# Performance work log

Measured on AMD Instinct MI355X. Metric: run time of the kernel, lower is better.

The kernel has to match this reference:

```python
import jax, jax.numpy as jnp
import numpy as np

TAU = 0.5


def _l2norm(x):
    # F.normalize(p=2, dim=1): x / max(||x||, eps) with eps=1e-12
    n = jnp.sqrt(jnp.sum(x * x, axis=1, keepdims=True))
    return x / jnp.maximum(n, 1e-12)


def setup_inputs() -> dict:
    key = jax.random.key(0)
    k1, k2 = jax.random.split(key)
    N, D = 8192, 512
    left = jax.random.normal(k1, (N, D), dtype=jnp.float32)
    right = jax.random.normal(k2, (N, D), dtype=jnp.float32)
    return {"left": left, "right": right}


def reference(left, right) -> jnp.ndarray:
    zl = _l2norm(left)
    zr = _l2norm(right)
    # [N, N] cosine-similarity matrices
    refl_sim = jnp.exp(jnp.matmul(zl, zl.T) / TAU)
    between_sim = jnp.exp(jnp.matmul(zl, zr.T) / TAU)
    between_diag = jnp.diagonal(between_sim)
    refl_diag = jnp.diagonal(refl_sim)
    denom = refl_sim.sum(axis=1) + between_sim.sum(axis=1) - refl_diag
    loss = -jnp.log(between_diag / denom)  # [N]
    return loss
```

## Files before the change

kernel.cpp:

```cpp
#include <hip/hip_runtime.h>

#define NROWS 8192
#define DDIM 512
#define ZROWS 16384
#define BM 256
#define BN 256
#define BK 64
#define KTILES (DDIM / BK)
#define NLR_BLOCKS 1024
#define NSYM_BLOCKS 528
#define NBLOCKS (NLR_BLOCKS + NSYM_BLOCKS)

typedef __attribute__((ext_vector_type(8))) short short8;
typedef __attribute__((ext_vector_type(4))) float f32x4;

__device__ __forceinline__ unsigned short f2bf(float f) {
  unsigned int u = __float_as_uint(f);
  u = (u + 0x7FFFu + ((u >> 16) & 1u)) >> 16;
  return (unsigned short)u;
}

__global__ __launch_bounds__(256) void nrm_kernel(const float* __restrict__ left,
                                                  const float* __restrict__ right,
                                                  unsigned short* __restrict__ Z,
                                                  float* __restrict__ dlr) {
  const int i = blockIdx.x;
  const int t = threadIdx.x;
  const float2 lv = ((const float2*)(left + (size_t)i * DDIM))[t];
  const float2 rv = ((const float2*)(right + (size_t)i * DDIM))[t];
  float ssl = lv.x * lv.x + lv.y * lv.y;
  float ssr = rv.x * rv.x + rv.y * rv.y;
  float slr = lv.x * rv.x + lv.y * rv.y;
#pragma unroll
  for (int m = 1; m < 64; m <<= 1) {
    ssl += __shfl_xor(ssl, m);
    ssr += __shfl_xor(ssr, m);
    slr += __shfl_xor(slr, m);
  }
  __shared__ float red[3][4];
  const int w = t >> 6;
  if ((t & 63) == 0) { red[0][w] = ssl; red[1][w] = ssr; red[2][w] = slr; }
  __syncthreads();
  ssl = red[0][0] + red[0][1] + red[0][2] + red[0][3];
  ssr = red[1][0] + red[1][1] + red[1][2] + red[1][3];
  slr = red[2][0] + red[2][1] + red[2][2] + red[2][3];
  const float invl = 1.0f / fmaxf(sqrtf(ssl), 1e-12f);
  const float invr = 1.0f / fmaxf(sqrtf(ssr), 1e-12f);
  if (t == 0) dlr[i] = slr * invl * invr;
  ushort2 zl2; zl2.x = f2bf(lv.x * invl); zl2.y = f2bf(lv.y * invl);
  ushort2 zr2; zr2.x = f2bf(rv.x * invr); zr2.y = f2bf(rv.y * invr);
  ((ushort2*)(Z + (size_t)i * DDIM))[t] = zl2;
  ((ushort2*)(Z + (size_t)(NROWS + i) * DDIM))[t] = zr2;
}

__global__ __launch_bounds__(512) void sim_kernel(const unsigned short* __restrict__ Z,
                                                  float* __restrict__ partial) {
  __shared__ __align__(16) unsigned short sA[2][BM * BK];
  __shared__ __align__(16) unsigned short sB[2][BN * BK];
  __shared__ float rsum[BM];
  __shared__ float csum[BM];

  int tm, tn; bool sym = false;
  {
    const int bid = blockIdx.x;
    if (bid < NLR_BLOCKS) {
      tm = bid >> 5; tn = 32 + (bid & 31);
    } else {
      const int b2 = bid - NLR_BLOCKS;
      int i = (int)(32.5f - sqrtf(32.5f * 32.5f - 2.0f * (float)b2));
      if (i < 0) i = 0; if (i > 31) i = 31;
      while (i > 0 && (32 * i - i * (i - 1) / 2) > b2) --i;
      while (i < 31 && (32 * (i + 1) - (i + 1) * i / 2) <= b2) ++i;
      tm = i; tn = i + (b2 - (32 * i - i * (i - 1) / 2));
      sym = (tn != tm);
    }
  }

  const int t = threadIdx.x;
  const int l = t & 63;
  const int w = t >> 6;
  const int wm = w >> 2;
  const int wn = w & 3;
  const int lr = l & 15;
  const int lk = l >> 4;

  f32x4 acc[8][4];
#pragma unroll
  for (int a = 0; a < 8; ++a)
#pragma unroll
    for (int b = 0; b < 4; ++b)
#pragma unroll
      for (int r = 0; r < 4; ++r) acc[a][b][r] = 0.0f;

  const unsigned short* Abase = Z + (size_t)tm * BM * DDIM;
  const unsigned short* Bbase = Z + (size_t)tn * BN * DDIM;

  const int srow = t >> 3;
  const int scol = ((t & 7) ^ (srow & 7)) * 8;

#define STAGE_AJ(bufi, k0, j)                                                     \
  __builtin_amdgcn_global_load_lds(                                               \
      (const __attribute__((address_space(1))) void*)(Abase +                     \
          (size_t)((j) * 64 + srow) * DDIM + (k0) + scol),                        \
      (__attribute__((address_space(3))) void*)(&sA[bufi][((j) * 512 + t) * 8]),  \
      16, 0, 0);
#define STAGE_BJ(bufi, k0, j)                                                     \
  __builtin_amdgcn_global_load_lds(                                               \
      (const __attribute__((address_space(1))) void*)(Bbase +                     \
          (size_t)((j) * 64 + srow) * DDIM + (k0) + scol),                        \
      (__attribute__((address_space(3))) void*)(&sB[bufi][((j) * 512 + t) * 8]),  \
      16, 0, 0);
#define STAGE_A02(b, k0) { STAGE_AJ(b, k0, 0) STAGE_AJ(b, k0, 2) }
#define STAGE_A13(b, k0) { STAGE_AJ(b, k0, 1) STAGE_AJ(b, k0, 3) }
#define STAGE_B01(b, k0) { STAGE_BJ(b, k0, 0) STAGE_BJ(b, k0, 1) }
#define STAGE_B23(b, k0) { STAGE_BJ(b, k0, 2) STAGE_BJ(b, k0, 3) }

  short8 af[4][2], ag[4][2], bf[4][2];

#define DS_A(dst, bufi, fmb)                                                       \
  _Pragma("unroll")                                                                \
  for (int fm = 0; fm < 4; ++fm)                                                   \
    _Pragma("unroll")                                                              \
    for (int ks = 0; ks < 2; ++ks) {                                               \
      const int row = wm * 128 + ((fmb) + fm) * 16 + lr;                           \
      dst[fm][ks] = *(const short8*)&sA[bufi][row * BK + ((ks * 4 + lk) ^ (lr & 7)) * 8]; \
    }

#define DS_B2(bufi, fnb)                                                           \
  _Pragma("unroll")                                                                \
  for (int fn = 0; fn < 2; ++fn)                                                   \
    _Pragma("unroll")                                                              \
    for (int ks = 0; ks < 2; ++ks) {                                               \
      const int row = wn * 64 + ((fnb) + fn) * 16 + lr;                            \
      bf[(fnb) + fn][ks] = *(const short8*)&sB[bufi][row * BK + ((ks * 4 + lk) ^ (lr & 7)) * 8]; \
    }

#define MFMA16(A, fmb, fnb)                                                        \
  __builtin_amdgcn_s_setprio(1);                                                   \
  _Pragma("unroll")                                                                \
  for (int ks = 0; ks < 2; ++ks)                                                   \
    _Pragma("unroll")                                                              \
    for (int fm = 0; fm < 4; ++fm)                                                 \
      _Pragma("unroll")                                                            \
      for (int fn = 0; fn < 2; ++fn)                                               \
        acc[(fmb) + fm][(fnb) + fn] =                                              \
            __builtin_amdgcn_mfma_f32_16x16x32_bf16(A[fm][ks], bf[(fnb) + fn][ks], \
                                                    acc[(fmb) + fm][(fnb) + fn],   \
                                                    0, 0, 0);                      \
  __builtin_amdgcn_s_setprio(0);

#define BARF  { __builtin_amdgcn_s_barrier(); asm volatile("" ::: "memory"); }
#define VM6   asm volatile("s_waitcnt vmcnt(6)" ::: "memory")
#define VM0   asm volatile("s_waitcnt vmcnt(0)" ::: "memory")

  STAGE_A02(0, 0); STAGE_A13(0, 0); STAGE_B01(0, 0); STAGE_B23(0, 0);
  STAGE_A02(1, BK); STAGE_B01(1, BK); STAGE_B23(1, BK);
  VM6;
  BARF;

#pragma unroll
  for (int it = 0; it < 4; ++it) {
    const int kt = 2 * it;
    DS_A(af, 0, 0); DS_B2(0, 0);
    STAGE_A13(1, (kt + 1) * BK);
    BARF;
    MFMA16(af, 0, 0);
    DS_B2(0, 2);
    if (kt + 2 < KTILES) STAGE_A02(0, (kt + 2) * BK);
    BARF;
    MFMA16(af, 0, 2);
    DS_A(ag, 0, 4);
    if (kt + 2 < KTILES) STAGE_B01(0, (kt + 2) * BK);
    BARF;
    MFMA16(ag, 4, 0);
    if (kt + 2 < KTILES) { STAGE_B23(0, (kt + 2) * BK); VM6; } else { VM0; }
    BARF;
    MFMA16(ag, 4, 2);
    DS_A(af, 1, 0); DS_B2(1, 0);
    if (kt + 2 < KTILES) STAGE_A13(0, (kt + 2) * BK);
    BARF;
    MFMA16(af, 0, 0);
    DS_B2(1, 2);
    if (kt + 3 < KTILES) STAGE_A02(1, (kt + 3) * BK);
    BARF;
    MFMA16(af, 0, 2);
    DS_A(ag, 1, 4);
    if (kt + 3 < KTILES) STAGE_B01(1, (kt + 3) * BK);
    BARF;
    MFMA16(ag, 4, 0);
    if (kt + 3 < KTILES) { STAGE_B23(1, (kt + 3) * BK); VM6; } else { VM0; }
    BARF;
    MFMA16(ag, 4, 2);
  }

  if (t < BM) { rsum[t] = 0.0f; csum[t] = 0.0f; }
  __syncthreads();
  float c0 = 0.0f, c1 = 0.0f, c2 = 0.0f, c3 = 0.0f;
#pragma unroll
  for (int fm = 0; fm < 8; ++fm) {
#pragma unroll
    for (int r = 0; r < 4; ++r) {
      float e0 = __expf(2.0f * acc[fm][0][r]);
      float e1 = __expf(2.0f * acc[fm][1][r]);
      float e2 = __expf(2.0f * acc[fm][2][r]);
      float e3 = __expf(2.0f * acc[fm][3][r]);
      float v = e0 + e1 + e2 + e3;
      v += __shfl_xor(v, 1);
      v += __shfl_xor(v, 2);
      v += __shfl_xor(v, 4);
      v += __shfl_xor(v, 8);
      if (lr == 0) atomicAdd(&rsum[wm * 128 + fm * 16 + lk * 4 + r], v);
      c0 += e0; c1 += e1; c2 += e2; c3 += e3;
    }
  }
  if (sym) {
    c0 += __shfl_xor(c0, 16); c0 += __shfl_xor(c0, 32);
    c1 += __shfl_xor(c1, 16); c1 += __shfl_xor(c1, 32);
    c2 += __shfl_xor(c2, 16); c2 += __shfl_xor(c2, 32);
    c3 += __shfl_xor(c3, 16); c3 += __shfl_xor(c3, 32);
    if (l < 16) {
      atomicAdd(&csum[wn * 64 +  0 + lr], c0);
      atomicAdd(&csum[wn * 64 + 16 + lr], c1);
      atomicAdd(&csum[wn * 64 + 32 + lr], c2);
      atomicAdd(&csum[wn * 64 + 48 + lr], c3);
    }
  }
  __syncthreads();
  if (t < BM) partial[(size_t)tn * NROWS + tm * BM + t] = rsum[t];
  if (sym && t < BM) partial[(size_t)tm * NROWS + tn * BM + t] = csum[t];
}

__global__ __launch_bounds__(256) void fin_kernel(const float* __restrict__ partial,
                                                  const float* __restrict__ dlr,
                                                  float* __restrict__ out) {
  const int i = blockIdx.x * 256 + threadIdx.x;
  float s = 0.0f;
#pragma unroll 8
  for (int p = 0; p < 64; ++p) s += partial[(size_t)p * NROWS + i];
  out[i] = logf(s - 7.38905609893065f) - 2.0f * dlr[i];
}

extern "C" void kernel_launch(void* const* d_in, const int* in_sizes, int n_in,
                              void* d_out, int out_size, void* d_ws, size_t ws_size,
                              hipStream_t stream) {
  const float* left = (const float*)d_in[0];
  const float* right = (const float*)d_in[1];
  float* out = (float*)d_out;

  unsigned short* Z = (unsigned short*)d_ws;
  char* p = (char*)d_ws + (size_t)ZROWS * DDIM * 2;
  float* dlr = (float*)p;
  float* partial = (float*)(p + (size_t)NROWS * 4);

  nrm_kernel<<<NROWS, 256, 0, stream>>>(left, right, Z, dlr);
  sim_kernel<<<NBLOCKS, 512, 0, stream>>>(Z, partial);
  fin_kernel<<<NROWS / 256, 256, 0, stream>>>(partial, dlr, out);
}
```

Baseline: 151.6 us.

## Simplify GEMM main loop to single-barrier double buffering per k-tile

Replaces the finely interleaved 8-phase schedule, where global-to-LDS loads for quarter-tiles were staged between MFMA groups with partial vmcnt waits and many barriers, with a simple double-buffer loop. Each iteration issues all loads for the next k-tile up front, computes the current tile, then waits for all loads and synchronises once. This cuts barrier count and code complexity, but the full vmcnt(0) wait and coarser issue may expose more memory latency and reduce overlap between loads and MFMA work.

```diff
diff --git a/kernel.cpp b/kernel.cpp
--- a/kernel.cpp
+++ b/kernel.cpp
@@ -110,10 +110,10 @@
           (size_t)((j) * 64 + srow) * DDIM + (k0) + scol),                        \
       (__attribute__((address_space(3))) void*)(&sB[bufi][((j) * 512 + t) * 8]),  \
       16, 0, 0);
-#define STAGE_A02(b, k0) { STAGE_AJ(b, k0, 0) STAGE_AJ(b, k0, 2) }
-#define STAGE_A13(b, k0) { STAGE_AJ(b, k0, 1) STAGE_AJ(b, k0, 3) }
-#define STAGE_B01(b, k0) { STAGE_BJ(b, k0, 0) STAGE_BJ(b, k0, 1) }
-#define STAGE_B23(b, k0) { STAGE_BJ(b, k0, 2) STAGE_BJ(b, k0, 3) }
+#define STAGE_ALL(b, k0) { STAGE_AJ(b, k0, 0) STAGE_AJ(b, k0, 1)                  \
+                           STAGE_AJ(b, k0, 2) STAGE_AJ(b, k0, 3)                  \
+                           STAGE_BJ(b, k0, 0) STAGE_BJ(b, k0, 1)                  \
+                           STAGE_BJ(b, k0, 2) STAGE_BJ(b, k0, 3) }
 
   short8 af[4][2], ag[4][2], bf[4][2];
 
@@ -150,47 +150,26 @@
   __builtin_amdgcn_s_setprio(0);
 
 #define BARF  { __builtin_amdgcn_s_barrier(); asm volatile("" ::: "memory"); }
-#define VM6   asm volatile("s_waitcnt vmcnt(6)" ::: "memory")
 #define VM0   asm volatile("s_waitcnt vmcnt(0)" ::: "memory")
 
-  STAGE_A02(0, 0); STAGE_A13(0, 0); STAGE_B01(0, 0); STAGE_B23(0, 0);
-  STAGE_A02(1, BK); STAGE_B01(1, BK); STAGE_B23(1, BK);
-  VM6;
+  STAGE_ALL(0, 0);
+  VM0;
   BARF;
 
 #pragma unroll
-  for (int it = 0; it < 4; ++it) {
-    const int kt = 2 * it;
-    DS_A(af, 0, 0); DS_B2(0, 0);
-    STAGE_A13(1, (kt + 1) * BK);
+  for (int kt = 0; kt < KTILES; ++kt) {
+    const int cur = kt & 1;
+    const int nxt = cur ^ 1;
+    if (kt + 1 < KTILES) STAGE_ALL(nxt, (kt + 1) * BK);
+    DS_A(af, cur, 0); DS_B2(cur, 0);
+    MFMA16(af, 0, 0);
+    DS_B2(cur, 2);
+    MFMA16(af, 0, 2);
+    DS_A(ag, cur, 4);
+    MFMA16(ag, 4, 0);
+    MFMA16(ag, 4, 2);
+    VM0;
     BARF;
-    MFMA16(af, 0, 0);
-    DS_B2(0, 2);
-    if (kt + 2 < KTILES) STAGE_A02(0, (kt + 2) * BK);
-    BARF;
-    MFMA16(af, 0, 2);
-    DS_A(ag, 0, 4);
-    if (kt + 2 < KTILES) STAGE_B01(0, (kt + 2) * BK);
-    BARF;
-    MFMA16(ag, 4, 0);
-    if (kt + 2 < KTILES) { STAGE_B23(0, (kt + 2) * BK); VM6; } else { VM0; }
-    BARF;
-    MFMA16(ag, 4, 2);
-    DS_A(af, 1, 0); DS_B2(1, 0);
-    if (kt + 2 < KTILES) STAGE_A13(0, (kt + 2) * BK);
-    BARF;
-    MFMA16(af, 0, 0);
-    DS_B2(1, 2);
-    if (kt + 3 < KTILES) STAGE_A02(1, (kt + 3) * BK);
-    BARF;
-    MFMA16(af, 0, 2);
-    DS_A(ag, 1, 4);
-    if (kt + 3 < KTILES) STAGE_B01(1, (kt + 3) * BK);
-    BARF;
-    MFMA16(ag, 4, 0);
-    if (kt + 3 < KTILES) { STAGE_B23(1, (kt + 3) * BK); VM6; } else { VM0; }
-    BARF;
-    MFMA16(ag, 4, 2);
   }
 
   if (t < BM) { rsum[t] = 0.0f; csum[t] = 0.0f; }
```

Result: slower. 155.0 us (+2.2%).
